# Optimization experiments

Measured on AMD Instinct MI355X. Metric: run time of the kernel, lower is better.

Reference implementation:

```python
import jax, jax.numpy as jnp
import numpy as np

B, C, H, W = 16, 64, 64, 64  # z_e shape; C == embedding_dim
K = 1024                     # num_embeddings
COMMITMENT_COST = 0.25
EPS = 1e-5


def setup_inputs() -> dict:
    key = jax.random.key(0)
    k1, k2 = jax.random.split(key)
    z_e = jax.random.normal(k1, (B, C, H, W), dtype=jnp.float32)
    # codebook init ~ U(-1/D, 1/D) as in the torch module
    emb_w = jax.random.uniform(k2, (K, C), dtype=jnp.float32, minval=-1.0 / C, maxval=1.0 / C)
    return {"z_e": z_e, "emb_w": emb_w}


def reference(z_e, emb_w):
    orig_dtype = z_e.dtype
    b, c, h, w = z_e.shape
    z = z_e.astype(jnp.float32)
    # per-channel std over (batch, h, w); computed under no_grad in torch -> stop_gradient
    std = jax.lax.stop_gradient(
        jnp.clip(jnp.std(z, axis=(0, 2, 3), keepdims=True, ddof=1), EPS, None)
    )
    z = z / std                                        # [b,c,h,w]
    zf = z.transpose(0, 2, 3, 1).reshape(-1, c)        # [N, c]
    ew = emb_w.astype(jnp.float32)                     # [K, c]
    # squared euclidean distances: ||z||^2 - 2 z.e + ||e||^2  -> [N, K]
    d = (
        jnp.sum(zf * zf, axis=1, keepdims=True)
        - 2.0 * (zf @ ew.T)
        + jnp.sum(ew * ew, axis=1)
    )
    idx = jnp.argmin(d, axis=1)                        # [N]
    z_q = ew[idx].reshape(b, h, w, c).transpose(0, 3, 1, 2)  # [b,c,h,w]
    z_sg = jax.lax.stop_gradient(z)
    commitment = COMMITMENT_COST * jnp.mean((z_sg - z_q) ** 2)
    codebook = jnp.mean((z_sg - z_q) ** 2)             # eval-mode codebook loss
    vq_loss = commitment + codebook
    z_q_st = (z + jax.lax.stop_gradient(z_q - z)).astype(orig_dtype)
    n_tokens = idx.shape[0]
    counts = jnp.zeros((K,), dtype=jnp.float32).at[idx].add(1.0)
    avg_probs = counts / n_tokens
    perplexity = jnp.exp(-jnp.sum(avg_probs * jnp.log(jnp.clip(avg_probs, 1e-10, None))))
    indices = idx.reshape(b, h, w)
    return z_q_st, vq_loss, perplexity, indices
```

## Files before the change

### kernel.cpp

```cpp
#include <hip/hip_runtime.h>
#include <math.h>
#include <float.h>

#define HW 4096
#define CHW 262144
#define NTOK 65536
#define NELEM 4194304

#define WS_LOSS 0
#define WS_PART 1024
#define WS_EE   2048
#define WS_E2   3072
#define WS_HIST 68608
#define WS_DONE 69632

#define EPSM 1.0e-4f

typedef __attribute__((ext_vector_type(8))) short bf16x8;
typedef __attribute__((ext_vector_type(4))) float f32x4;

__device__ __forceinline__ unsigned short f2bf(float x) {
  unsigned u = __float_as_uint(x);
  u += 0x7FFFu + ((u >> 16) & 1u);
  return (unsigned short)(u >> 16);
}
__device__ __forceinline__ float bf2f(unsigned short h) {
  return __uint_as_float(((unsigned)h) << 16);
}
__device__ __forceinline__ void gload_lds16(const unsigned short* g, unsigned short* l) {
  __builtin_amdgcn_global_load_lds(
      (const __attribute__((address_space(1))) unsigned int*)g,
      (__attribute__((address_space(3))) unsigned int*)l, 16, 0, 0);
}

__global__ __launch_bounds__(1024) void k_pre(const float* __restrict__ z,
                                              const float* __restrict__ emb,
                                              double* __restrict__ part,
                                              unsigned short* __restrict__ e2g,
                                              float* __restrict__ eeg,
                                              int* __restrict__ hist,
                                              int* __restrict__ done) {
  __shared__ double rs[16], rs2[16];
  int tid = threadIdx.x;
  int blk = blockIdx.x;
  if (blk == 0 && tid == 0) *done = 0;
  if (blk < 256) {
    int c = blk & 63, q = blk >> 6;
    double s = 0.0, s2 = 0.0;
    const float* base = z + (size_t)c * HW;
    #pragma unroll
    for (int jj = 0; jj < 4; ++jj) {
      int bb = (q << 2) + jj;
      float4 v = *(const float4*)(base + (size_t)bb * CHW + (tid << 2));
      s  += (double)v.x + (double)v.y + (double)v.z + (double)v.w;
      s2 += (double)v.x * v.x + (double)v.y * v.y + (double)v.z * v.z + (double)v.w * v.w;
    }
    for (int o = 32; o > 0; o >>= 1) {
      s += __shfl_down(s, o, 64);
      s2 += __shfl_down(s2, o, 64);
    }
    int wv = tid >> 6, ln = tid & 63;
    if (ln == 0) { rs[wv] = s; rs2[wv] = s2; }
    __syncthreads();
    if (tid == 0) {
      double S = 0.0, S2 = 0.0;
      #pragma unroll
      for (int w = 0; w < 16; ++w) { S += rs[w]; S2 += rs2[w]; }
      part[(c << 2) + q] = S;
      part[256 + (c << 2) + q] = S2;
    }
  } else {
    int ct = blk - 256;
    if (ct == 0) hist[tid] = 0;
    int k0 = ct << 6;
    int code = tid >> 4, c4 = tid & 15;
    float4 v = *(const float4*)(emb + (size_t)((k0 + code) << 6) + (c4 << 2));
    unsigned short h0 = f2bf(v.x), h1 = f2bf(v.y), h2 = f2bf(v.z), h3 = f2bf(v.w);
    unsigned short l0 = f2bf(v.x - bf2f(h0)), l1 = f2bf(v.y - bf2f(h1));
    unsigned short l2 = f2bf(v.z - bf2f(h2)), l3 = f2bf(v.w - bf2f(h3));
    int jL = (c4 >> 1) & 3;
    int e = (c4 & 1) << 2;
    int cH = code >> 4, cL = code & 15;
    size_t base = (size_t)ct * 8192 + cH * 512 + jL * 128 + cL * 8 + e;
    int jHh = c4 >> 3;
    *(uint2*)(e2g + base + (size_t)jHh * 2048) =
        make_uint2((unsigned)h0 | ((unsigned)h1 << 16), (unsigned)h2 | ((unsigned)h3 << 16));
    *(uint2*)(e2g + base + (size_t)(2 + jHh) * 2048) =
        make_uint2((unsigned)l0 | ((unsigned)l1 << 16), (unsigned)l2 | ((unsigned)l3 << 16));
    if (tid < 64) {
      const float* er = emb + (size_t)((k0 + tid) << 6);
      float s = 0.f;
      #pragma unroll
      for (int c = 0; c < 64; ++c) s = fmaf(er[c], er[c], s);
      eeg[k0 + tid] = s;
    }
  }
}

__global__ __launch_bounds__(256, 2) void k_vq(
    const float* __restrict__ z_e, const float* __restrict__ emb,
    const double* __restrict__ part, const float* __restrict__ eeg,
    const unsigned short* __restrict__ e2g,
    float* __restrict__ out_zq, float* __restrict__ out_idx,
    float* __restrict__ loss_part, int* __restrict__ done,
    float* __restrict__ out_scalars, int* __restrict__ hist) {
  __shared__ unsigned short A2[8192];
  __shared__ unsigned short B2[8192];
  __shared__ float sEE[1024];
  __shared__ float sRstd[64];
  __shared__ double rl[4], rh[4];
  __shared__ int lastFlag;
  float* hs1 = (float*)A2;
  float* hs2 = (float*)A2 + 256;
  float* hs3 = (float*)A2 + 512;
  int*   hk1 = (int*)A2 + 768;
  int*   hk2 = (int*)A2 + 1024;
  int*   skf = (int*)A2 + 1280;
  int*   mk2f = (int*)A2 + 1344;
  int*   pairL = (int*)A2 + 1408;
  int*   fullL = (int*)A2 + 1472;
  int*   cntB = (int*)A2 + 1536;
  int*   cntC = (int*)A2 + 1537;
  float* sred = (float*)A2 + 1540;
  float* zf   = (float*)A2 + 1544;
  float* fbd4 = (float*)A2 + 1608;
  int*   fbk4 = (int*)A2 + 1612;

  int tid = threadIdx.x;
  int lane = tid & 63;
  int wv = tid >> 6;
  int blk = blockIdx.x;
  int b = blk >> 6;
  int s0 = (blk & 63) << 6;

  {
    const unsigned short* gsrc = e2g + wv * 512 + (lane << 3);
    unsigned short* ldst = B2 + wv * 512;
    #pragma unroll
    for (int rr = 0; rr < 4; ++rr)
      gload_lds16(gsrc + rr * 2048, ldst + rr * 2048);
  }

  ((float4*)sEE)[tid] = ((const float4*)eeg)[tid];

  if (tid < 64) {
    double S = 0.0, S2 = 0.0;
    #pragma unroll
    for (int q = 0; q < 4; ++q) {
      S += part[(tid << 2) + q];
      S2 += part[256 + (tid << 2) + q];
    }
    const double N = (double)NTOK;
    double var = (S2 - S * S / N) / (N - 1.0);
    float sd = fmaxf((float)sqrt(var), 1e-5f);
    sRstd[tid] = 1.0f / sd;
  }
  __syncthreads();

  {
    int t = tid & 63, q = tid >> 6;
    int half = q >> 1, jl0 = (q & 1) << 1;
    const float* zsrc = z_e + (size_t)b * CHW + (size_t)(q << 4) * HW + s0 + t;
    unsigned hw_[8], lw_[8];
    #pragma unroll
    for (int cc = 0; cc < 16; ++cc) {
      float v = zsrc[(size_t)cc * HW] * sRstd[(q << 4) + cc];
      unsigned short h = f2bf(v);
      unsigned short l = f2bf(v - bf2f(h));
      if (cc & 1) { hw_[cc >> 1] |= ((unsigned)h) << 16; lw_[cc >> 1] |= ((unsigned)l) << 16; }
      else        { hw_[cc >> 1] = h;                    lw_[cc >> 1] = l; }
    }
    int base = (t >> 4) * 512 + (t & 15) * 8;
    #pragma unroll
    for (int u = 0; u < 2; ++u) {
      *(uint4*)(A2 + half * 2048 + base + (jl0 + u) * 128) =
          make_uint4(hw_[4 * u], hw_[4 * u + 1], hw_[4 * u + 2], hw_[4 * u + 3]);
      *(uint4*)(A2 + (2 + half) * 2048 + base + (jl0 + u) * 128) =
          make_uint4(lw_[4 * u], lw_[4 * u + 1], lw_[4 * u + 2], lw_[4 * u + 3]);
    }
  }
  __syncthreads();

  int quad = lane >> 4, l15 = lane & 15;

  bf16x8 afc[4][4];
  #pragma unroll
  for (int j = 0; j < 4; ++j)
    #pragma unroll
    for (int mt = 0; mt < 4; ++mt)
      afc[j][mt] = *(const bf16x8*)(A2 + j * 2048 + mt * 512 + quad * 128 + l15 * 8);
  __syncthreads();

  float ts1[16], ts2[16], ts3[16];
  int tk1[16], tk2[16];
  #pragma unroll
  for (int i = 0; i < 16; ++i) { ts1[i] = FLT_MAX; ts2[i] = FLT_MAX; ts3[i] = FLT_MAX; tk1[i] = 0; tk2[i] = 0; }

  const int aJH[8] = {0, 1, 2, 3, 0, 1, 2, 3};
  const int bJH[8] = {0, 1, 0, 1, 2, 3, 2, 3};

  #pragma unroll 1
  for (int ct = 0; ct < 16; ++ct) {
    const unsigned short* bb = (ct & 1) ? A2 : B2;
    if (ct < 15) {
      const unsigned short* gsrc = e2g + (size_t)(ct + 1) * 8192 + wv * 512 + (lane << 3);
      unsigned short* ldst = (((ct + 1) & 1) ? A2 : B2) + wv * 512;
      #pragma unroll
      for (int rr = 0; rr < 4; ++rr)
        gload_lds16(gsrc + rr * 2048, ldst + rr * 2048);
      asm volatile("s_waitcnt vmcnt(4)" ::: "memory");
    } else {
      asm volatile("s_waitcnt vmcnt(0)" ::: "memory");
    }
    float ee0 = sEE[(ct << 6) + (wv << 4) + l15];

    f32x4 acc[4];
    #pragma unroll
    for (int mt = 0; mt < 4; ++mt) acc[mt] = (f32x4)(0.f);

    __builtin_amdgcn_s_setprio(1);
    #pragma unroll
    for (int s = 0; s < 8; ++s) {
      bf16x8 bfr = *(const bf16x8*)(bb + bJH[s] * 2048 + wv * 512 + quad * 128 + l15 * 8);
      #pragma unroll
      for (int mt = 0; mt < 4; ++mt)
        acc[mt] = __builtin_amdgcn_mfma_f32_16x16x32_bf16(afc[aJH[s]][mt], bfr, acc[mt], 0, 0, 0);
    }
    __builtin_amdgcn_s_setprio(0);

    int kc = (ct << 6) + (wv << 4) + l15;
    #pragma unroll
    for (int mt = 0; mt < 4; ++mt) {
      #pragma unroll
      for (int r = 0; r < 4; ++r) {
        float sv = fmaf(-2.0f, acc[mt][r], ee0);
        int sl = (mt << 2) + r;
        bool lt1 = sv < ts1[sl];
        bool lt2 = sv < ts2[sl];
        ts3[sl] = fminf(fmaxf(sv, ts2[sl]), ts3[sl]);
        tk2[sl] = lt1 ? tk1[sl] : (lt2 ? kc : tk2[sl]);
        ts2[sl] = fminf(fmaxf(sv, ts1[sl]), ts2[sl]);
        tk1[sl] = lt1 ? kc : tk1[sl];
        ts1[sl] = fminf(sv, ts1[sl]);
      }
    }
  }
  __syncthreads();

  #pragma unroll
  for (int m = 1; m <= 8; m <<= 1) {
    #pragma unroll
    for (int sl = 0; sl < 16; ++sl) {
      float ob1 = __shfl_xor(ts1[sl], m, 64); int oq1 = __shfl_xor(tk1[sl], m, 64);
      float ob2 = __shfl_xor(ts2[sl], m, 64); int oq2 = __shfl_xor(tk2[sl], m, 64);
      float ob3 = __shfl_xor(ts3[sl], m, 64);
      bool t1 = (ts1[sl] < ob1) || (ts1[sl] == ob1 && tk1[sl] < oq1);
      float o1 = t1 ? ts1[sl] : ob1; int ok1 = t1 ? tk1[sl] : oq1;
      float aH = t1 ? ts2[sl] : ts1[sl]; int aHk = t1 ? tk2[sl] : tk1[sl]; float aH2 = t1 ? ts3[sl] : ts2[sl];
      float bH = t1 ? ob1 : ob2;         int bHk = t1 ? oq1 : oq2;         float bH2 = t1 ? ob2 : ob3;
      bool t2 = (aH < bH) || (aH == bH && aHk < bHk);
      float o2 = t2 ? aH : bH; int ok2 = t2 ? aHk : bHk;
      float aI = t2 ? aH2 : aH;
      float bI = t2 ? bH : bH2;
      ts1[sl] = o1; tk1[sl] = ok1; ts2[sl] = o2; tk2[sl] = ok2; ts3[sl] = fminf(aI, bI);
    }
  }
  if (tid == 0) { *cntB = 0; *cntC = 0; }
  if (l15 == 0) {
    #pragma unroll
    for (int mt = 0; mt < 4; ++mt)
      #pragma unroll
      for (int r = 0; r < 4; ++r) {
        int t = (mt << 4) + (quad << 2) + r;
        int sl = (mt << 2) + r;
        hs1[(wv << 6) + t] = ts1[sl]; hs2[(wv << 6) + t] = ts2[sl]; hs3[(wv << 6) + t] = ts3[sl];
        hk1[(wv << 6) + t] = tk1[sl]; hk2[(wv << 6) + t] = tk2[sl];
      }
  }
  __syncthreads();

  if (tid < 64) {
    float a1 = hs1[tid], a2 = hs2[tid], a3 = hs3[tid];
    int e1 = hk1[tid], e2v = hk2[tid];
    #pragma unroll
    for (int w = 1; w < 4; ++w) {
      float b1 = hs1[(w << 6) + tid], b2 = hs2[(w << 6) + tid], b3 = hs3[(w << 6) + tid];
      int f1 = hk1[(w << 6) + tid], f2 = hk2[(w << 6) + tid];
      bool t1 = (a1 < b1) || (a1 == b1 && e1 < f1);
      float o1 = t1 ? a1 : b1; int ok1 = t1 ? e1 : f1;
      float aH = t1 ? a2 : a1; int aHk = t1 ? e2v : e1; float aH2 = t1 ? a3 : a2;
      float bH = t1 ? b1 : b2; int bHk = t1 ? f1 : f2; float bH2 = t1 ? b2 : b3;
      bool t2 = (aH < bH) || (aH == bH && aHk < bHk);
      a1 = o1; e1 = ok1;
      a2 = t2 ? aH : bH; e2v = t2 ? aHk : bHk;
      a3 = fminf(t2 ? aH2 : aH, t2 ? bH : bH2);
    }
    skf[tid] = e1;
    mk2f[tid] = e2v;
    if (a2 - a1 <= EPSM) {
      if (a3 - a1 > EPSM) { int p = atomicAdd(cntB, 1); pairL[p] = tid; }
      else                { int p = atomicAdd(cntC, 1); fullL[p] = tid; }
    }
  }
  __syncthreads();

  int nB = *cntB, nC = *cntC;

  if (tid < nB) {
    int t = pairL[tid];
    int ka = skf[t], kb = mk2f[t];
    const float* za = z_e + (size_t)b * CHW + s0 + t;
    const float* ea = emb + ((size_t)ka << 6);
    const float* ebp = emb + ((size_t)kb << 6);
    float zz = 0.f, da = 0.f, db = 0.f;
    #pragma unroll
    for (int c = 0; c < 64; ++c) {
      float zv = za[(size_t)c * HW] * sRstd[c];
      zz = fmaf(zv, zv, zz);
      da = fmaf(ea[c], zv, da);
      db = fmaf(ebp[c], zv, db);
    }
    float d1 = (zz - 2.0f * da) + eeg[ka];
    float d2 = (zz - 2.0f * db) + eeg[kb];
    if (d2 < d1 || (d2 == d1 && kb < ka)) skf[t] = kb;
  }
  __syncthreads();

  for (int i = 0; i < nC; ++i) {
    int t = fullL[i];
    if (tid < 64) zf[tid] = z_e[(size_t)b * CHW + (size_t)tid * HW + s0 + t] * sRstd[tid];
    __syncthreads();
    const float4* zf4 = (const float4*)zf;
    const float* er0 = emb + ((size_t)(tid << 2) << 6);
    float zz = 0.f;
    float dot[4] = {0.f, 0.f, 0.f, 0.f};
    #pragma unroll
    for (int c4 = 0; c4 < 16; ++c4) {
      float4 zv = zf4[c4];
      zz = fmaf(zv.x, zv.x, zz); zz = fmaf(zv.y, zv.y, zz);
      zz = fmaf(zv.z, zv.z, zz); zz = fmaf(zv.w, zv.w, zz);
      #pragma unroll
      for (int j = 0; j < 4; ++j) {
        float4 ev = *(const float4*)(er0 + (j << 6) + (c4 << 2));
        dot[j] = fmaf(ev.x, zv.x, dot[j]);
        dot[j] = fmaf(ev.y, zv.y, dot[j]);
        dot[j] = fmaf(ev.z, zv.z, dot[j]);
        dot[j] = fmaf(ev.w, zv.w, dot[j]);
      }
    }
    float bdl = FLT_MAX; int bkl = 0;
    #pragma unroll
    for (int j = 0; j < 4; ++j) {
      float dd = (zz - 2.0f * dot[j]) + eeg[(tid << 2) + j];
      if (dd < bdl) { bdl = dd; bkl = (tid << 2) + j; }
    }
    #pragma unroll
    for (int m = 1; m <= 32; m <<= 1) {
      float od = __shfl_xor(bdl, m, 64);
      int   ok = __shfl_xor(bkl, m, 64);
      if (od < bdl || (od == bdl && ok < bkl)) { bdl = od; bkl = ok; }
    }
    if (lane == 0) { fbd4[wv] = bdl; fbk4[wv] = bkl; }
    __syncthreads();
    if (tid == 0) {
      float bb2 = fbd4[0]; int kk2 = fbk4[0];
      #pragma unroll
      for (int w = 1; w < 4; ++w)
        if (fbd4[w] < bb2 || (fbd4[w] == bb2 && fbk4[w] < kk2)) { bb2 = fbd4[w]; kk2 = fbk4[w]; }
      skf[t] = kk2;
    }
    __syncthreads();
  }
  __syncthreads();

  if (tid < 64) {
    int k = skf[tid];
    out_idx[(blk << 6) + tid] = (float)k;
    atomicAdd(&hist[k], 1);
  }

  {
    int t = tid & 63;
    int g = tid >> 6;
    int kq = skf[t];
    const float* eq = emb + ((size_t)kq << 6) + (g << 4);
    const float* zb2 = z_e + (size_t)b * CHW + (size_t)(g << 4) * HW + s0 + t;
    float* ob = out_zq + (size_t)b * CHW + (size_t)(g << 4) * HW + s0 + t;
    float lsum = 0.f;
    #pragma unroll
    for (int j4 = 0; j4 < 4; ++j4) {
      float4 ev = *(const float4*)(eq + (j4 << 2));
      #pragma unroll
      for (int u = 0; u < 4; ++u) {
        int jj = (j4 << 2) + u;
        float zv = zb2[(size_t)jj * HW] * sRstd[(g << 4) + jj];
        float e = (&ev.x)[u];
        float df = zv - e;
        lsum = fmaf(df, df, lsum);
        ob[(size_t)jj * HW] = zv + (e - zv);
      }
    }
    for (int o = 32; o > 0; o >>= 1) lsum += __shfl_down(lsum, o, 64);
    if (lane == 0) sred[wv] = lsum;
  }
  __syncthreads();

  if (tid == 0) {
    loss_part[blk] = sred[0] + sred[1] + sred[2] + sred[3];
    __threadfence();
    int prev = atomicAdd(done, 1);
    lastFlag = (prev == 1023);
  }
  __syncthreads();
  if (!lastFlag) return;

  double ls = (double)loss_part[tid] + (double)loss_part[tid + 256]
            + (double)loss_part[tid + 512] + (double)loss_part[tid + 768];
  double hsum = 0.0;
  #pragma unroll
  for (int jj = 0; jj < 4; ++jj) {
    float p = (float)hist[tid + (jj << 8)] * (1.0f / 65536.0f);
    float lg = logf(fmaxf(p, 1e-10f));
    hsum += (double)(p * lg);
  }
  for (int o = 32; o > 0; o >>= 1) {
    ls += __shfl_down(ls, o, 64);
    hsum += __shfl_down(hsum, o, 64);
  }
  if (lane == 0) { rl[wv] = ls; rh[wv] = hsum; }
  __syncthreads();
  if (tid == 0) {
    double L = rl[0] + rl[1] + rl[2] + rl[3];
    double Hn = rh[0] + rh[1] + rh[2] + rh[3];
    float m = (float)(L / (double)NELEM);
    out_scalars[0] = 0.25f * m + m;
    out_scalars[1] = expf((float)(-Hn));
  }
}

extern "C" void kernel_launch(void* const* d_in, const int* in_sizes, int n_in,
                              void* d_out, int out_size, void* d_ws, size_t ws_size,
                              hipStream_t stream) {
  const float* z_e = (const float*)d_in[0];
  const float* emb = (const float*)d_in[1];
  float* ws = (float*)d_ws;
  float* loss_part = ws + WS_LOSS;
  double* part = (double*)(ws + WS_PART);
  float* eeg = ws + WS_EE;
  unsigned short* e2g = (unsigned short*)(ws + WS_E2);
  int* hist = (int*)(ws + WS_HIST);
  int* done = (int*)(ws + WS_DONE);

  float* out = (float*)d_out;
  float* out_zq = out;
  float* out_scalars = out + NELEM;
  float* out_idx = out + NELEM + 2;

  k_pre<<<272, 1024, 0, stream>>>(z_e, emb, part, e2g, eeg, hist, done);
  k_vq<<<1024, 256, 0, stream>>>(z_e, emb, part, eeg, e2g, out_zq, out_idx,
                                 loss_part, done, out_scalars, hist);
}
```

Measured before the change: 203.6 us.

## Hoist z_e loads early and replace per-wave vmcnt waits with block barriers

The z_e loads for the bf16 split are now issued before the std-reduction barrier, so their latency overlaps that reduction. A second set of z_e loads for the epilogue is issued right after the distance loop, ahead of the shuffle reductions, instead of being re-read inside the output loop. The explicit s_waitcnt vmcnt instructions and the s_setprio hints around the MFMA loop are removed. In their place, a __syncthreads at the end of each codebook tile iteration orders the double-buffered LDS reads and writes. This trades extra block barriers and higher register pressure for more overlapped global loads and cross-wave ordering of the buffers.

New measurement: 195.4 us. 4.0% less time.

```diff
diff --git a/kernel.cpp b/kernel.cpp
--- a/kernel.cpp
+++ b/kernel.cpp
@@ -132,6 +132,7 @@
   int blk = blockIdx.x;
   int b = blk >> 6;
   int s0 = (blk & 63) << 6;
+  int t63 = tid & 63, q4 = tid >> 6;
 
   {
     const unsigned short* gsrc = e2g + wv * 512 + (lane << 3);
@@ -142,6 +143,13 @@
   }
 
   ((float4*)sEE)[tid] = ((const float4*)eeg)[tid];
+
+  float zr[16];
+  {
+    const float* zsrc = z_e + (size_t)b * CHW + (size_t)(q4 << 4) * HW + s0 + t63;
+    #pragma unroll
+    for (int cc = 0; cc < 16; ++cc) zr[cc] = zsrc[(size_t)cc * HW];
+  }
 
   if (tid < 64) {
     double S = 0.0, S2 = 0.0;
@@ -158,19 +166,17 @@
   __syncthreads();
 
   {
-    int t = tid & 63, q = tid >> 6;
-    int half = q >> 1, jl0 = (q & 1) << 1;
-    const float* zsrc = z_e + (size_t)b * CHW + (size_t)(q << 4) * HW + s0 + t;
+    int half = q4 >> 1, jl0 = (q4 & 1) << 1;
     unsigned hw_[8], lw_[8];
     #pragma unroll
     for (int cc = 0; cc < 16; ++cc) {
-      float v = zsrc[(size_t)cc * HW] * sRstd[(q << 4) + cc];
+      float v = zr[cc] * sRstd[(q4 << 4) + cc];
       unsigned short h = f2bf(v);
       unsigned short l = f2bf(v - bf2f(h));
       if (cc & 1) { hw_[cc >> 1] |= ((unsigned)h) << 16; lw_[cc >> 1] |= ((unsigned)l) << 16; }
       else        { hw_[cc >> 1] = h;                    lw_[cc >> 1] = l; }
     }
-    int base = (t >> 4) * 512 + (t & 15) * 8;
+    int base = (t63 >> 4) * 512 + (t63 & 15) * 8;
     #pragma unroll
     for (int u = 0; u < 2; ++u) {
       *(uint4*)(A2 + half * 2048 + base + (jl0 + u) * 128) =
@@ -208,9 +214,6 @@
       #pragma unroll
       for (int rr = 0; rr < 4; ++rr)
         gload_lds16(gsrc + rr * 2048, ldst + rr * 2048);
-      asm volatile("s_waitcnt vmcnt(4)" ::: "memory");
-    } else {
-      asm volatile("s_waitcnt vmcnt(0)" ::: "memory");
     }
     float ee0 = sEE[(ct << 6) + (wv << 4) + l15];
 
@@ -218,7 +221,6 @@
     #pragma unroll
     for (int mt = 0; mt < 4; ++mt) acc[mt] = (f32x4)(0.f);
 
-    __builtin_amdgcn_s_setprio(1);
     #pragma unroll
     for (int s = 0; s < 8; ++s) {
       bf16x8 bfr = *(const bf16x8*)(bb + bJH[s] * 2048 + wv * 512 + quad * 128 + l15 * 8);
@@ -226,7 +228,6 @@
       for (int mt = 0; mt < 4; ++mt)
         acc[mt] = __builtin_amdgcn_mfma_f32_16x16x32_bf16(afc[aJH[s]][mt], bfr, acc[mt], 0, 0, 0);
     }
-    __builtin_amdgcn_s_setprio(0);
 
     int kc = (ct << 6) + (wv << 4) + l15;
     #pragma unroll
@@ -244,8 +245,16 @@
         ts1[sl] = fminf(sv, ts1[sl]);
       }
     }
-  }
-  __syncthreads();
+    if (ct < 15) __syncthreads();
+  }
+  __syncthreads();
+
+  float zr2[16];
+  {
+    const float* z2 = z_e + (size_t)b * CHW + (size_t)(q4 << 4) * HW + s0 + t63;
+    #pragma unroll
+    for (int cc = 0; cc < 16; ++cc) zr2[cc] = z2[(size_t)cc * HW];
+  }
 
   #pragma unroll
   for (int m = 1; m <= 8; m <<= 1) {
@@ -380,12 +389,9 @@
   }
 
   {
-    int t = tid & 63;
-    int g = tid >> 6;
-    int kq = skf[t];
-    const float* eq = emb + ((size_t)kq << 6) + (g << 4);
-    const float* zb2 = z_e + (size_t)b * CHW + (size_t)(g << 4) * HW + s0 + t;
-    float* ob = out_zq + (size_t)b * CHW + (size_t)(g << 4) * HW + s0 + t;
+    int kq = skf[t63];
+    const float* eq = emb + ((size_t)kq << 6) + (q4 << 4);
+    float* ob = out_zq + (size_t)b * CHW + (size_t)(q4 << 4) * HW + s0 + t63;
     float lsum = 0.f;
     #pragma unroll
     for (int j4 = 0; j4 < 4; ++j4) {
@@ -393,7 +399,7 @@
       #pragma unroll
       for (int u = 0; u < 4; ++u) {
         int jj = (j4 << 2) + u;
-        float zv = zb2[(size_t)jj * HW] * sRstd[(g << 4) + jj];
+        float zv = zr2[jj] * sRstd[(q4 << 4) + jj];
         float e = (&ev.x)[u];
         float df = zv - e;
         lsum = fmaf(df, df, lsum);
```
